# Performance work log

Measured on AMD Instinct MI355X. Metric: run time of the kernel, lower is better.

Reference implementation:

```python
import jax, jax.numpy as jnp
import numpy as np

N, T, S, A, L, Z = 128, 100, 128, 32, 1024, 1024


def _gru(x, h0, Wih, Whh, bih, bhh):
    # x: [T, N, in], h0: [N, H]; torch nn.GRU cell math
    xg = jnp.einsum('tni,gi->tng', x, Wih) + bih  # [T, N, 3H]

    def step(h, xg_t):
        hg = h @ Whh.T + bhh
        xr, xz, xn = jnp.split(xg_t, 3, axis=-1)
        hr, hz, hn = jnp.split(hg, 3, axis=-1)
        r = jax.nn.sigmoid(xr + hr)
        z = jax.nn.sigmoid(xz + hz)
        n = jnp.tanh(xn + r * hn)
        h_new = (1.0 - z) * n + z * h
        return h_new, h_new

    hT, out = jax.lax.scan(step, h0, xg)
    return out, hT  # out: [T, N, H]


def _roll_batch(x, shifts):
    # per-sample left-roll along time: out[n, t] = x[n, (t + shifts[n]) % T]
    Tt = x.shape[1]
    idx = (jnp.arange(Tt)[None, :] + shifts[:, None]) % Tt  # [N, T]
    return jnp.take_along_axis(x, idx[:, :, None], axis=1)


def setup_inputs() -> dict:
    key = jax.random.key(0)
    ks = jax.random.split(key, 40)
    # ragged valid lengths in [50, 98]; zero tails trigger split-point detection
    lengths = jax.random.randint(ks[0], (N,), 50, 99)
    s = jax.random.normal(ks[1], (N, T, S), jnp.float32)
    valid = (jnp.arange(T)[None, :] < lengths[:, None])[:, :, None]
    s = jnp.where(valid, s, 0.0)
    inp = {
        's': s,
        'a': jax.random.normal(ks[2], (N, T, A), jnp.float32),
        's_final': jax.random.normal(ks[3], (N, S), jnp.float32),
        's_next': jax.random.normal(ks[4], (N, T, S), jnp.float32),
        'eps': jax.random.normal(ks[5], (N, Z), jnp.float32),
    }
    shapes = {
        'enc_Wih': (3 * L, S + A), 'enc_Whh': (3 * L, L), 'enc_bih': (3 * L,), 'enc_bhh': (3 * L,),
        'mu_W': (Z, L), 'mu_b': (Z,), 'lv_W': (Z, L), 'lv_b': (Z,),
        'st1_W': (128, L), 'st1_b': (128,), 'st2_W': (64, 128), 'st2_b': (64,),
        'st3_W': (S, 64), 'st3_b': (S,),
        'dec_Wih': (3 * Z, A), 'dec_Whh': (3 * Z, Z), 'dec_bih': (3 * Z,), 'dec_bhh': (3 * Z,),
        'd1_W': (128, Z), 'd1_b': (128,), 'd2_W': (64, 128), 'd2_b': (64,),
        'd3_W': (S, 64), 'd3_b': (S,),
    }
    for i, (name, shp) in enumerate(shapes.items()):
        fan_in = shp[-1] if len(shp) > 1 else 1024
        bound = 1.0 / np.sqrt(fan_in)
        inp[name] = jax.random.uniform(ks[6 + i], shp, jnp.float32, -bound, bound)
    return inp


def reference(s, a, s_final, s_next, eps,
              enc_Wih, enc_Whh, enc_bih, enc_bhh,
              mu_W, mu_b, lv_W, lv_b,
              st1_W, st1_b, st2_W, st2_b, st3_W, st3_b,
              dec_Wih, dec_Whh, dec_bih, dec_bhh,
              d1_W, d1_b, d2_W, d2_b, d3_W, d3_b):
    Nn, Tt = s.shape[0], s.shape[1]
    # split points: first t where s[n, t+1] is all-zero (padding tail)
    is_zero = jnp.all(s == 0.0, axis=-1)                    # [N, T]
    end = jnp.argmax(is_zero[:, 1:], axis=1)                # end_points
    start = end + 2                                         # start_points
    # encoder (initial hidden = ones, per original)
    x = jnp.concatenate([s, a], axis=-1).transpose(1, 0, 2)  # [T, N, S+A]
    h0 = jnp.ones((Nn, enc_Whh.shape[-1]), dtype=s.dtype)
    enc_out, _ = _gru(x, h0, enc_Wih, enc_Whh, enc_bih, enc_bhh)  # [T, N, L]
    enc_out = enc_out.transpose(1, 0, 2)                          # [N, T, L]
    hf = jnp.take_along_axis(enc_out, end[:, None, None], axis=1)[:, 0, :]  # [N, L]
    # reparametrize
    mu = hf @ mu_W.T + mu_b
    logvar = hf @ lv_W.T + lv_b
    emb = mu + jnp.exp(logvar / 2.0) * eps
    # final-state head (computed but not used in the returned loss, per original)
    x1 = jax.nn.relu(emb @ st1_W.T + st1_b)
    x2 = jax.nn.relu(x1 @ st2_W.T + st2_b)
    s_final_hat = x2 @ st3_W.T + st3_b
    # decoder: per-sample roll of actions by -start, initial hidden = embeddings
    a_roll = _roll_batch(a, start)
    dec_out, _ = _gru(a_roll.transpose(1, 0, 2), emb, dec_Wih, dec_Whh, dec_bih, dec_bhh)  # [T, N, Z]
    y1 = jax.nn.relu(dec_out @ d1_W.T + d1_b)
    y2 = jax.nn.relu(y1 @ d2_W.T + d2_b)
    s_next_hat = (y2 @ d3_W.T + d3_b).transpose(1, 0, 2)    # [N, T, S]
    # masked L1 loss on rolled next-states: error[n, :T-start[n]]
    s_next_roll = _roll_batch(s_next, start)
    err = jnp.abs(s_next_roll - s_next_hat)
    mask = (jnp.arange(Tt)[None, :] < (Tt - start)[:, None]).astype(err.dtype)
    loss = jnp.sum(err * mask[:, :, None])
    return loss.reshape(1, 1)
```

## Files before the change

### kernel.cpp

```cpp
#include <hip/hip_runtime.h>
#include <math.h>

#define NN_ 128
#define TT  100
#define SS  128
#define AA  32
#define LL  1024
#define NBLK 256
#define HRS  1034


typedef __attribute__((ext_vector_type(8))) short bf16x8;
typedef __attribute__((ext_vector_type(4))) float f32x4;
typedef __attribute__((ext_vector_type(4))) int   i32x4;

__device__ __forceinline__ float sigmoidf_(float x) { return 1.0f / (1.0f + expf(-x)); }
__device__ __forceinline__ unsigned short f2bf(float x) {
    union { float f; unsigned u; } v; v.f = x;
    return (unsigned short)((v.u + 0x7fffu + ((v.u >> 16) & 1u)) >> 16);
}

__device__ __forceinline__ i32x4 ldg16(const unsigned short* p) {
    i32x4 r; asm volatile("global_load_dwordx4 %0, %1, off sc0 sc1"
                          : "=&v"(r) : "v"((unsigned long long)p));
    return r;
}
__device__ __forceinline__ void stg16(unsigned short* p, bf16x8 v) {
    union { bf16x8 h; i32x4 i; } u; u.h = v;
    asm volatile("global_store_dwordx4 %0, %1, off sc0 sc1"
                 :: "v"((unsigned long long)p), "v"(u.i) : "memory");
}
__device__ __forceinline__ void st2(unsigned short* p, unsigned short v) {
    asm volatile("global_store_short %0, %1, off sc0 sc1"
                 :: "v"((unsigned long long)p), "v"((unsigned)v) : "memory");
}
__device__ __forceinline__ int aload(const int* p) {
    return __hip_atomic_load(p, __ATOMIC_RELAXED, __HIP_MEMORY_SCOPE_AGENT);
}
__device__ __forceinline__ void astore(int* p, int v) {
    __hip_atomic_store(p, v, __ATOMIC_RELAXED, __HIP_MEMORY_SCOPE_AGENT);
}

struct PParams {
    const float *s, *a, *s_next, *eps;
    const float *eWih, *eWhh, *ebih, *ebhh;
    const float *muW, *mub, *lvW, *lvb;
    const float *dWih, *dWhh, *dbih, *dbhh;
    const float *d1W, *d1b, *d2W, *d2b, *d3W, *d3b;
    int *bar;
    int *endv, *startv, *limitv;
    unsigned short *hencAb, *hencBb, *hdecAb, *hdecBb, *hf_bf;
    unsigned short *eWih_b, *eWhh_b, *dWih_b, *dWhh_b, *mlW_b, *xenc_b, *adec_b;
    unsigned short *d1Wb, *d2Wb, *d3Wb;
    unsigned short *y1b, *y2b;
    float *loss;
};

__device__ __forceinline__ void stage_h32p(const unsigned short* __restrict__ src,
                                           const int* __restrict__ sperm,
                                           unsigned short* hstage, int tid) {
    i32x4 v[16];
    const int p = tid >> 7, col = (tid & 127) * 8;
    #pragma unroll
    for (int k = 0; k < 16; ++k) {
        const int row = sperm[p + 2 * k];
        v[k] = ldg16(src + (size_t)row * LL + col);
    }
    asm volatile("s_waitcnt vmcnt(0)" ::: "memory");
    #pragma unroll
    for (int k = 0; k < 16; ++k)
        *(i32x4*)&hstage[(p + 2 * k) * HRS + col] = v[k];
}

__device__ void gbar_global(int* bar, int bid, int tid, int gen) {
    __syncthreads();
    if (tid == 0) {
        if (aload(bar + 132) == 0) {
            const int g8 = bid & 7;
            int pos = __hip_atomic_fetch_add(bar + g8 * 16, 1, __ATOMIC_RELAXED, __HIP_MEMORY_SCOPE_AGENT);
            if (pos + 1 == (NBLK / 8) * gen) {
                int mp = __hip_atomic_fetch_add(bar + 128, 1, __ATOMIC_RELAXED, __HIP_MEMORY_SCOPE_AGENT);
                if (mp + 1 == 8 * gen) {
                    for (int b = 0; b < NBLK; ++b)
                        astore(bar + 144 + b * 16, gen);
                }
            }
            int it = 0;
            while (aload(bar + 144 + bid * 16) < gen) {
                __builtin_amdgcn_s_sleep(1);
                if (++it > 4000000) { astore(bar + 132, 1); break; }
            }
        }
    }
    __syncthreads();
}

__device__ void gbar_group(int* gb, int* brk, int lbid, int tid, int gen, int* sbrk) {
    asm volatile("s_waitcnt vmcnt(0)" ::: "memory");
    __syncthreads();
    if (tid == 0) {
        const int s = lbid & 3;
        int pos = __hip_atomic_fetch_add(gb + s * 16, 1, __ATOMIC_RELAXED, __HIP_MEMORY_SCOPE_AGENT);
        if (pos + 1 == 16 * gen) {
            int mp = __hip_atomic_fetch_add(gb + 64, 1, __ATOMIC_RELAXED, __HIP_MEMORY_SCOPE_AGENT);
            if (mp + 1 == 4 * gen)
                astore(gb + 80, gen);
        }
        if (*sbrk == 0) {
            int it = 0;
            while (aload(gb + 80) < gen) {
                __builtin_amdgcn_s_sleep(1);
                if (((++it) & 2047) == 0) {
                    if (aload(brk)) { *sbrk = 1; break; }
                    if (it > 2000000) { astore(brk, 1); *sbrk = 1; break; }
                }
            }
        }
    }
    __syncthreads();
}

__global__ void init_kernel(int* bar, float* loss) {
    for (int i = threadIdx.x; i < 5632; i += 256) bar[i] = 0;
    if (threadIdx.x == 0) loss[0] = 0.0f;
}

template<int XK, bool IS_DEC>
__device__ void gru_tile(const int* __restrict__ sperm, const int jb, const int tid,
    const unsigned short* __restrict__ h_bf, unsigned short* __restrict__ ho_bf,
    const unsigned short* __restrict__ Whh_b, const unsigned short* __restrict__ Wih_b,
    const unsigned short* __restrict__ x_bf,
    const float* __restrict__ bih, const float* __restrict__ bhh,
    const int* __restrict__ endv, unsigned short* __restrict__ hf_bf,
    int t, f32x4 (&red)[2][4][64], unsigned short* hstage, unsigned short* trb,
    f32x4& hold)
{
    const int lane = tid & 63, w = tid >> 6;
    const int nh = w & 1, kh = w >> 1;
    const int m = lane & 15, quad = lane >> 4;
    const int jcol = jb + m;

    stage_h32p(h_bf, sperm, hstage, tid);
    __syncthreads();

    f32x4 accr{}, accz{}, acchn{}, accxn{};

    {
        const int arow = (nh * 16 + m) * HRS + quad * 8;
        const unsigned short* brp = Whh_b + (size_t)(0 * LL + jcol) * LL + quad * 8;
        const unsigned short* bzp = Whh_b + (size_t)(1 * LL + jcol) * LL + quad * 8;
        const unsigned short* bnp = Whh_b + (size_t)(2 * LL + jcol) * LL + quad * 8;
        #pragma unroll 4
        for (int c = kh * 16; c < kh * 16 + 16; ++c) {
            const int k0 = c * 32;
            bf16x8 av = *(const bf16x8*)&hstage[arow + k0];
            bf16x8 br = *(const bf16x8*)(brp + k0);
            bf16x8 bz = *(const bf16x8*)(bzp + k0);
            bf16x8 bn = *(const bf16x8*)(bnp + k0);
            accr  = __builtin_amdgcn_mfma_f32_16x16x32_bf16(av, br, accr, 0, 0, 0);
            accz  = __builtin_amdgcn_mfma_f32_16x16x32_bf16(av, bz, accz, 0, 0, 0);
            acchn = __builtin_amdgcn_mfma_f32_16x16x32_bf16(av, bn, acchn, 0, 0, 0);
        }
    }
    {
        const int XC = XK / 32, XC0 = (XC + 1) / 2;
        const size_t xstride = IS_DEC ? (size_t)(50 * AA) : (size_t)(TT * (SS + AA));
        const int nphys = sperm[nh * 16 + m];
        const unsigned short* xp  = x_bf + (size_t)nphys * xstride + (size_t)t * XK + quad * 8;
        const unsigned short* brp = Wih_b + (size_t)(0 * LL + jcol) * XK + quad * 8;
        const unsigned short* bzp = Wih_b + (size_t)(1 * LL + jcol) * XK + quad * 8;
        const unsigned short* bnp = Wih_b + (size_t)(2 * LL + jcol) * XK + quad * 8;
        #pragma unroll
        for (int c = (kh ? XC0 : 0); c < (kh ? XC : XC0); ++c) {
            const int k0 = c * 32;
            bf16x8 av = *(const bf16x8*)(xp + k0);
            bf16x8 br = *(const bf16x8*)(brp + k0);
            bf16x8 bz = *(const bf16x8*)(bzp + k0);
            bf16x8 bn = *(const bf16x8*)(bnp + k0);
            accr  = __builtin_amdgcn_mfma_f32_16x16x32_bf16(av, br, accr, 0, 0, 0);
            accz  = __builtin_amdgcn_mfma_f32_16x16x32_bf16(av, bz, accz, 0, 0, 0);
            accxn = __builtin_amdgcn_mfma_f32_16x16x32_bf16(av, bn, accxn, 0, 0, 0);
        }
    }
    if (kh == 1) {
        red[nh][0][lane] = accr;  red[nh][1][lane] = accz;
        red[nh][2][lane] = acchn; red[nh][3][lane] = accxn;
    }
    __syncthreads();
    if (kh == 0) {
        accr  += red[nh][0][lane];  accz  += red[nh][1][lane];
        acchn += red[nh][2][lane];  accxn += red[nh][3][lane];
        const float br_  = bih[jcol] + bhh[jcol];
        const float bz_  = bih[LL + jcol] + bhh[LL + jcol];
        const float bxn_ = bih[2 * LL + jcol];
        const float bhn_ = bhh[2 * LL + jcol];
        unsigned short* tr = trb + nh * (16 * 24);
        #pragma unroll
        for (int i = 0; i < 4; ++i) {
            const int n = sperm[nh * 16 + quad * 4 + i];
            float r = sigmoidf_(accr[i] + br_);
            float z = sigmoidf_(accz[i] + bz_);
            float g = tanhf(accxn[i] + bxn_ + r * (acchn[i] + bhn_));
            float hn = (1.0f - z) * g + z * hold[i];
            hold[i] = hn;
            unsigned short hb = f2bf(hn);
            tr[(quad * 4 + i) * 24 + m] = hb;
            if (!IS_DEC) { if (endv[n] == t) st2(hf_bf + (size_t)n * LL + jcol, hb); }
        }
        if (lane < 32) {
            const int nl = lane >> 1, jh = lane & 1;
            bf16x8 vv = *(const bf16x8*)&tr[nl * 24 + jh * 8];
            stg16(ho_bf + (size_t)sperm[nh * 16 + nl] * LL + jb + jh * 8, vv);
        }
    }
}

__device__ void emb_tile(const PParams& P, const int* __restrict__ sperm, const int jb,
                         const int tid, f32x4 (&red)[2][4][64], unsigned short* hstage,
                         unsigned short* trb, f32x4& hold)
{
    const int lane = tid & 63, w = tid >> 6;
    const int nh = w & 1, kh = w >> 1;
    const int m = lane & 15, quad = lane >> 4;
    const int jcol = jb + m;

    stage_h32p(P.hf_bf, sperm, hstage, tid);
    __syncthreads();

    f32x4 accm{}, accl{};
    const int arow = (nh * 16 + m) * HRS + quad * 8;
    const unsigned short* bmp = P.mlW_b + (size_t)jcol * LL + quad * 8;
    const unsigned short* blp = P.mlW_b + (size_t)(LL + jcol) * LL + quad * 8;
    #pragma unroll 4
    for (int c = kh * 16; c < kh * 16 + 16; ++c) {
        const int k0 = c * 32;
        bf16x8 av = *(const bf16x8*)&hstage[arow + k0];
        bf16x8 bm = *(const bf16x8*)(bmp + k0);
        bf16x8 bl = *(const bf16x8*)(blp + k0);
        accm = __builtin_amdgcn_mfma_f32_16x16x32_bf16(av, bm, accm, 0, 0, 0);
        accl = __builtin_amdgcn_mfma_f32_16x16x32_bf16(av, bl, accl, 0, 0, 0);
    }
    if (kh == 1) { red[nh][0][lane] = accm; red[nh][1][lane] = accl; }
    __syncthreads();
    if (kh == 0) {
        accm += red[nh][0][lane]; accl += red[nh][1][lane];
        unsigned short* tr = trb + nh * (16 * 24);
        #pragma unroll
        for (int i = 0; i < 4; ++i) {
            const int n = sperm[nh * 16 + quad * 4 + i];
            float mu = accm[i] + P.mub[jcol];
            float lv = accl[i] + P.lvb[jcol];
            float e = mu + expf(0.5f * lv) * P.eps[(size_t)n * LL + jcol];
            hold[i] = e;
            tr[(quad * 4 + i) * 24 + m] = f2bf(e);
        }
        if (lane < 32) {
            const int nl = lane >> 1, jh = lane & 1;
            bf16x8 vv = *(const bf16x8*)&tr[nl * 24 + jh * 8];
            stg16(P.hdecAb + (size_t)sperm[nh * 16 + nl] * LL + jb + jh * 8, vv);
        }
    }
}

__device__ void y1_tile(const PParams& P, int t, int tid,
                        const unsigned short* __restrict__ hstage,
                        unsigned short* __restrict__ y1cur)
{
    if (tid >= 64) return;
    const int m16 = tid & 15, quad = tid >> 4;
    const int rb = (t & 1) * 16, cb = (t >> 1) * 16;
    f32x4 acc{};
    const int abase = (rb + m16) * HRS + quad * 8;
    const unsigned short* bp = P.d1Wb + (size_t)(cb + m16) * LL + quad * 8;
    #pragma unroll 4
    for (int ch = 0; ch < 32; ++ch) {
        bf16x8 av = *(const bf16x8*)&hstage[abase + ch * 32];
        bf16x8 bv = *(const bf16x8*)(bp + ch * 32);
        acc = __builtin_amdgcn_mfma_f32_16x16x32_bf16(av, bv, acc, 0, 0, 0);
    }
    const float b = P.d1b[cb + m16];
    #pragma unroll
    for (int i = 0; i < 4; ++i)
        st2(y1cur + (rb + quad * 4 + i) * 128 + cb + m16, f2bf(fmaxf(acc[i] + b, 0.0f)));
}
__device__ void y2_tile(const PParams& P, int t, int tid,
                        const unsigned short* __restrict__ y1prev,
                        unsigned short* __restrict__ y2cur)
{
    if (tid >= 64) return;
    const int m16 = tid & 15, quad = tid >> 4;
    const int rb = (t & 1) * 16, cb = (t >> 1) * 16;
    i32x4 a4[4];
    #pragma unroll
    for (int ch = 0; ch < 4; ++ch)
        a4[ch] = ldg16(y1prev + (size_t)(rb + m16) * 128 + ch * 32 + quad * 8);
    asm volatile("s_waitcnt vmcnt(0)" ::: "memory");
    f32x4 acc{};
    #pragma unroll
    for (int ch = 0; ch < 4; ++ch) {
        union { i32x4 i; bf16x8 h; } u; u.i = a4[ch];
        bf16x8 bv = *(const bf16x8*)(P.d2Wb + (size_t)(cb + m16) * 128 + ch * 32 + quad * 8);
        acc = __builtin_amdgcn_mfma_f32_16x16x32_bf16(u.h, bv, acc, 0, 0, 0);
    }
    const float b = P.d2b[cb + m16];
    #pragma unroll
    for (int i = 0; i < 4; ++i)
        st2(y2cur + (rb + quad * 4 + i) * 64 + cb + m16, f2bf(fmaxf(acc[i] + b, 0.0f)));
}
__device__ void y3_loss(const PParams& P, const int* __restrict__ sperm, int t, int tid,
                        const unsigned short* __restrict__ y2prev, int ti, float& lossacc)
{
    if (tid >= 64) return;
    const int m16 = tid & 15, quad = tid >> 4;
    const int rb = (t & 1) * 16, cb = (t >> 1) * 16;
    i32x4 a2[2];
    #pragma unroll
    for (int ch = 0; ch < 2; ++ch)
        a2[ch] = ldg16(y2prev + (size_t)(rb + m16) * 64 + ch * 32 + quad * 8);
    asm volatile("s_waitcnt vmcnt(0)" ::: "memory");
    f32x4 acc{};
    #pragma unroll
    for (int ch = 0; ch < 2; ++ch) {
        union { i32x4 i; bf16x8 h; } u; u.i = a2[ch];
        bf16x8 bv = *(const bf16x8*)(P.d3Wb + (size_t)(cb + m16) * 64 + ch * 32 + quad * 8);
        acc = __builtin_amdgcn_mfma_f32_16x16x32_bf16(u.h, bv, acc, 0, 0, 0);
    }
    const int col = cb + m16;
    const float b = P.d3b[col];
    #pragma unroll
    for (int i = 0; i < 4; ++i) {
        const int n = sperm[rb + quad * 4 + i];
        if (ti < P.limitv[n]) {
            int trw = ti + P.startv[n]; if (trw >= TT) trw -= TT;
            float v = P.s_next[(size_t)n * TT * SS + (size_t)trw * SS + col];
            lossacc += fabsf(v - (acc[i] + b));
        }
    }
}

__global__ __launch_bounds__(256, 2)
void persist(PParams P)
{
    __shared__ __align__(16) unsigned short hstage[32 * HRS];
    __shared__ __align__(16) char shu[9728];
    __shared__ int sperm[32];
    __shared__ int mint, sME, sML, sbrk;
    f32x4 (&red)[2][4][64] = *(f32x4 (*)[2][4][64])(shu);
    unsigned short* trb = (unsigned short*)(shu + 8192);
    const int bid = blockIdx.x, tid = threadIdx.x;
    const int g = bid & 3, lbid = bid >> 2;
    const int jb = lbid * 16;
    int* gb = P.bar + 4608 + g * 128;
    int* brk = P.bar + 132;

    {
        const long N0 = 3072L * 160, N1 = N0 + 3072L * 1024, N2 = N1 + 3072L * 32,
                   N3 = N2 + 3072L * 1024, N4 = N3 + 1048576L, N5 = N4 + 1048576L,
                   N6 = N5 + 128L * 100 * 160, N7 = N6 + 131072L, N8 = N7 + 8192L,
                   N9 = N8 + 8192L;
        for (long i = (long)bid * 256 + tid; i < N9; i += (long)NBLK * 256) {
            if (i < N0)      P.eWih_b[i]      = f2bf(P.eWih[i]);
            else if (i < N1) P.eWhh_b[i - N0] = f2bf(P.eWhh[i - N0]);
            else if (i < N2) P.dWih_b[i - N1] = f2bf(P.dWih[i - N1]);
            else if (i < N3) P.dWhh_b[i - N2] = f2bf(P.dWhh[i - N2]);
            else if (i < N4) P.mlW_b[i - N3]  = f2bf(P.muW[i - N3]);
            else if (i < N5) P.mlW_b[1048576L + (i - N4)] = f2bf(P.lvW[i - N4]);
            else if (i < N6) {
                long j = i - N5;
                int  k = (int)(j % 160);
                long nt = j / 160;
                int  t = (int)(nt % 100), n = (int)(nt / 100);
                float v = (k < SS) ? P.s[(size_t)n * TT * SS + (size_t)t * SS + k]
                                   : P.a[(size_t)n * TT * AA + (size_t)t * AA + (k - SS)];
                P.xenc_b[j] = f2bf(v);
            }
            else if (i < N7) P.d1Wb[i - N6] = f2bf(P.d1W[i - N6]);
            else if (i < N8) P.d2Wb[i - N7] = f2bf(P.d2W[i - N7]);
            else             P.d3Wb[i - N8] = f2bf(P.d3W[i - N8]);
        }
    }
    if (bid < NN_) {
        const int n = bid;
        if (tid == 0) mint = TT - 1;
        __syncthreads();
        int t = tid + 1;
        if (t < TT && tid < 128) {
            const float* row = P.s + (size_t)n * TT * SS + (size_t)t * SS;
            bool allz = true;
            for (int i = 0; i < SS; ++i) { if (row[i] != 0.0f) { allz = false; break; } }
            if (allz) atomicMin(&mint, t);
        }
        __syncthreads();
        const int m = mint, st = m + 1;
        if (tid == 0) { P.endv[n] = m - 1; P.startv[n] = st; P.limitv[n] = TT - 1 - m; }
        for (int idx = tid; idx < LL; idx += 256)
            P.hencAb[(size_t)n * LL + idx] = 0x3F80;
        for (int idx = tid; idx < 50 * AA; idx += 256) {
            int i = idx >> 5, k = idx & 31;
            int tr = i + st; if (tr >= TT) tr -= TT;
            P.adec_b[(size_t)n * (50 * AA) + idx] =
                f2bf(P.a[(size_t)n * TT * AA + (size_t)tr * AA + k]);
        }
    }
    __syncthreads();
    if (tid == 0) __threadfence();
    gbar_global(P.bar, bid, tid, 1);
    if (tid == 0) __threadfence();
    __syncthreads();

    {
        int* keys = (int*)shu;
        if (tid < 128) keys[tid] = P.endv[tid];
        if (tid == 0) sbrk = 0;
        __syncthreads();
        if (tid < 128) {
            const int k = keys[tid];
            int r = 0;
            for (int j = 0; j < 128; ++j) {
                const int kj = keys[j];
                r += (kj < k) | ((kj == k) & (j < tid));
            }
            if (r >= g * 32 && r < g * 32 + 32) sperm[r - g * 32] = tid;
        }
        __syncthreads();
    }

    int ME, ML;
    {
        int lv = 0, ev = 0;
        if (tid < 32) { const int n = sperm[tid]; lv = P.limitv[n]; ev = P.endv[n]; }
        if (tid < 64) {
            for (int off = 16; off >= 1; off >>= 1) {
                lv = max(lv, __shfl_down(lv, off));
                ev = max(ev, __shfl_down(ev, off));
            }
            if (tid == 0) { sML = lv; sME = ev; }
        }
        __syncthreads();
        ML = sML; ME = sME;
        __syncthreads();
    }

    f32x4 hold = { 1.0f, 1.0f, 1.0f, 1.0f };
    float lossacc = 0.0f;
    int ggen = 0;

    for (int t = 0; t <= ME; ++t) {
        const unsigned short* hib = (t & 1) ? P.hencBb : P.hencAb;
        unsigned short*       hob = (t & 1) ? P.hencAb : P.hencBb;
        gru_tile<160, false>(sperm, jb, tid, hib, hob,
                             P.eWhh_b, P.eWih_b, P.xenc_b, P.ebih, P.ebhh,
                             P.endv, P.hf_bf, t, red, hstage, trb, hold);
        gbar_group(gb, brk, lbid, tid, ++ggen, &sbrk);
    }

    emb_tile(P, sperm, jb, tid, red, hstage, trb, hold);
    gbar_group(gb, brk, lbid, tid, ++ggen, &sbrk);

    unsigned short* y1g = P.y1b + (size_t)g * 2 * 32 * 128;
    unsigned short* y2g = P.y2b + (size_t)g * 2 * 32 * 64;
    for (int i = 0; i <= ML + 2; ++i) {
        const unsigned short* hib = (i & 1) ? P.hdecBb : P.hdecAb;
        if (i < ML) {
            unsigned short* hob = (i & 1) ? P.hdecAb : P.hdecBb;
            gru_tile<32, true>(sperm, jb, tid, hib, hob,
                               P.dWhh_b, P.dWih_b, P.adec_b, P.dbih, P.dbhh,
                               nullptr, nullptr, i, red, hstage, trb, hold);
        } else if (i == ML && lbid >= 48) {
            stage_h32p(hib, sperm, hstage, tid);
            __syncthreads();
        }
        if (lbid >= 48) {
            if (i >= 1 && i <= ML)
                y1_tile(P, lbid - 48, tid, hstage, y1g + (size_t)(i & 1) * 32 * 128);
        } else if (lbid >= 32 && lbid < 40) {
            if (i >= 2 && i <= ML + 1)
                y2_tile(P, lbid - 32, tid, y1g + (size_t)((i & 1) ^ 1) * 32 * 128,
                        y2g + (size_t)(i & 1) * 32 * 64);
        } else if (lbid < 16) {
            if (i >= 3)
                y3_loss(P, sperm, lbid, tid, y2g + (size_t)((i & 1) ^ 1) * 32 * 64,
                        i - 3, lossacc);
        }
        gbar_group(gb, brk, lbid, tid, ++ggen, &sbrk);
    }

    if (lbid < 16 && tid < 64) {
        for (int off = 32; off >= 1; off >>= 1) lossacc += __shfl_down(lossacc, off);
        if (tid == 0) atomicAdd(P.loss, lossacc);
    }
}

extern "C" void kernel_launch(void* const* d_in, const int* in_sizes, int n_in,
                              void* d_out, int out_size, void* d_ws, size_t ws_size,
                              hipStream_t stream) {
    PParams P;
    P.s      = (const float*)d_in[0];
    P.a      = (const float*)d_in[1];
    P.s_next = (const float*)d_in[3];
    P.eps    = (const float*)d_in[4];
    P.eWih   = (const float*)d_in[5];
    P.eWhh   = (const float*)d_in[6];
    P.ebih   = (const float*)d_in[7];
    P.ebhh   = (const float*)d_in[8];
    P.muW    = (const float*)d_in[9];
    P.mub    = (const float*)d_in[10];
    P.lvW    = (const float*)d_in[11];
    P.lvb    = (const float*)d_in[12];
    P.dWih   = (const float*)d_in[19];
    P.dWhh   = (const float*)d_in[20];
    P.dbih   = (const float*)d_in[21];
    P.dbhh   = (const float*)d_in[22];
    P.d1W    = (const float*)d_in[23];
    P.d1b    = (const float*)d_in[24];
    P.d2W    = (const float*)d_in[25];
    P.d2b    = (const float*)d_in[26];
    P.d3W    = (const float*)d_in[27];
    P.d3b    = (const float*)d_in[28];
    P.loss   = (float*)d_out;

    char* p = (char*)d_ws;
    P.bar    = (int*)p;                    p += 24576;
    P.endv   = (int*)p;                    p += 512;
    P.startv = (int*)p;                    p += 512;
    P.limitv = (int*)p;                    p += 512;
    p += 2560;
    P.hencAb = (unsigned short*)p;         p += 128 * 1024 * 2;
    P.hencBb = (unsigned short*)p;         p += 128 * 1024 * 2;
    P.hdecAb = (unsigned short*)p;         p += 128 * 1024 * 2;
    P.hdecBb = (unsigned short*)p;         p += 128 * 1024 * 2;
    P.hf_bf  = (unsigned short*)p;         p += 128 * 1024 * 2;
    P.eWih_b = (unsigned short*)p;         p += 3072 * 160 * 2;
    P.eWhh_b = (unsigned short*)p;         p += 3072 * 1024 * 2;
    P.dWih_b = (unsigned short*)p;         p += 3072 * 32 * 2;
    P.dWhh_b = (unsigned short*)p;         p += 3072 * 1024 * 2;
    P.mlW_b  = (unsigned short*)p;         p += 2048 * 1024 * 2;
    P.xenc_b = (unsigned short*)p;         p += 128 * 100 * 160 * 2;
    P.adec_b = (unsigned short*)p;         p += 128 * 50 * 32 * 2;
    P.d1Wb   = (unsigned short*)p;         p += 128 * 1024 * 2;
    P.d2Wb   = (unsigned short*)p;         p += 64 * 128 * 2;
    P.d3Wb   = (unsigned short*)p;         p += 128 * 64 * 2;
    P.y1b    = (unsigned short*)p;         p += 4 * 2 * 32 * 128 * 2;
    P.y2b    = (unsigned short*)p;         p += 4 * 2 * 32 * 64 * 2;

    hipLaunchKernelGGL(init_kernel, dim3(1), dim3(256), 0, stream, P.bar, P.loss);
    hipLaunchKernelGGL(persist, dim3(NBLK), dim3(256), 0, stream, P);
}
```

Measured before the change: 1.760 ms.

## Split grid barrier and overlap next-step input projection with barrier wait

The group barrier is split into separate arrive and wait phases. The input-to-hidden MFMA projection for the next timestep now runs between them, taking it off the serial recurrent critical path. The projection results are carried in registers and used as the starting accumulators for the hidden-state matmul. Scheduling barriers are also added after load waits in the y-tiles. The cost is extra live registers and possible register pressure.

Result: faster. 1.643 ms (-6.6%).

```diff
diff --git a/kernel.cpp b/kernel.cpp
--- a/kernel.cpp
+++ b/kernel.cpp
@@ -95,7 +95,7 @@
     __syncthreads();
 }
 
-__device__ void gbar_group(int* gb, int* brk, int lbid, int tid, int gen, int* sbrk) {
+__device__ void gbar_arrive(int* gb, int lbid, int tid, int gen) {
     asm volatile("s_waitcnt vmcnt(0)" ::: "memory");
     __syncthreads();
     if (tid == 0) {
@@ -106,14 +106,16 @@
             if (mp + 1 == 4 * gen)
                 astore(gb + 80, gen);
         }
-        if (*sbrk == 0) {
-            int it = 0;
-            while (aload(gb + 80) < gen) {
-                __builtin_amdgcn_s_sleep(1);
-                if (((++it) & 2047) == 0) {
-                    if (aload(brk)) { *sbrk = 1; break; }
-                    if (it > 2000000) { astore(brk, 1); *sbrk = 1; break; }
-                }
+    }
+}
+__device__ void gbar_wait(int* gb, int* brk, int tid, int gen, int* sbrk) {
+    if (tid == 0 && *sbrk == 0) {
+        int it = 0;
+        while (aload(gb + 80) < gen) {
+            __builtin_amdgcn_s_sleep(1);
+            if (((++it) & 2047) == 0) {
+                if (aload(brk)) { *sbrk = 1; break; }
+                if (it > 2000000) { astore(brk, 1); *sbrk = 1; break; }
             }
         }
     }
@@ -126,24 +128,53 @@
 }
 
 template<int XK, bool IS_DEC>
-__device__ void gru_tile(const int* __restrict__ sperm, const int jb, const int tid,
-    const unsigned short* __restrict__ h_bf, unsigned short* __restrict__ ho_bf,
-    const unsigned short* __restrict__ Whh_b, const unsigned short* __restrict__ Wih_b,
-    const unsigned short* __restrict__ x_bf,
-    const float* __restrict__ bih, const float* __restrict__ bhh,
-    const int* __restrict__ endv, unsigned short* __restrict__ hf_bf,
-    int t, f32x4 (&red)[2][4][64], unsigned short* hstage, unsigned short* trb,
-    f32x4& hold)
+__device__ __forceinline__ void x_part(const PParams& P, const int* __restrict__ sperm,
+    const int jb, const int tid, int t, f32x4& axr, f32x4& axz, f32x4& axn)
 {
     const int lane = tid & 63, w = tid >> 6;
     const int nh = w & 1, kh = w >> 1;
     const int m = lane & 15, quad = lane >> 4;
     const int jcol = jb + m;
+    const unsigned short* Wih_b = IS_DEC ? P.dWih_b : P.eWih_b;
+    const unsigned short* x_bf  = IS_DEC ? P.adec_b : P.xenc_b;
+    f32x4 r{}, z{}, n{};
+    const int XC = XK / 32, XC0 = (XC + 1) / 2;
+    const size_t xstride = IS_DEC ? (size_t)(50 * AA) : (size_t)(TT * (SS + AA));
+    const unsigned short* xp  = x_bf + (size_t)sperm[nh * 16 + m] * xstride + (size_t)t * XK + quad * 8;
+    const unsigned short* brp = Wih_b + (size_t)(0 * LL + jcol) * XK + quad * 8;
+    const unsigned short* bzp = Wih_b + (size_t)(1 * LL + jcol) * XK + quad * 8;
+    const unsigned short* bnp = Wih_b + (size_t)(2 * LL + jcol) * XK + quad * 8;
+    #pragma unroll
+    for (int c = (kh ? XC0 : 0); c < (kh ? XC : XC0); ++c) {
+        const int k0 = c * 32;
+        bf16x8 av = *(const bf16x8*)(xp + k0);
+        bf16x8 br = *(const bf16x8*)(brp + k0);
+        bf16x8 bz = *(const bf16x8*)(bzp + k0);
+        bf16x8 bn = *(const bf16x8*)(bnp + k0);
+        r = __builtin_amdgcn_mfma_f32_16x16x32_bf16(av, br, r, 0, 0, 0);
+        z = __builtin_amdgcn_mfma_f32_16x16x32_bf16(av, bz, z, 0, 0, 0);
+        n = __builtin_amdgcn_mfma_f32_16x16x32_bf16(av, bn, n, 0, 0, 0);
+    }
+    axr = r; axz = z; axn = n;
+}
+
+template<bool IS_DEC>
+__device__ void gru_tile(const PParams& P, const int* __restrict__ sperm, const int jb,
+    const int tid, const unsigned short* __restrict__ h_bf,
+    unsigned short* __restrict__ ho_bf, const unsigned short* __restrict__ Whh_b,
+    const float* __restrict__ bih, const float* __restrict__ bhh, int t,
+    f32x4 (&red)[2][4][64], unsigned short* hstage, unsigned short* trb, f32x4& hold,
+    const f32x4 axr, const f32x4 axz, const f32x4 axn)
+{
+    const int lane = tid & 63, w = tid >> 6;
+    const int nh = w & 1, kh = w >> 1;
+    const int m = lane & 15, quad = lane >> 4;
+    const int jcol = jb + m;
 
     stage_h32p(h_bf, sperm, hstage, tid);
     __syncthreads();
 
-    f32x4 accr{}, accz{}, acchn{}, accxn{};
+    f32x4 accr = axr, accz = axz, acchn{}, accxn = axn;
 
     {
         const int arow = (nh * 16 + m) * HRS + quad * 8;
@@ -160,26 +191,6 @@
             accr  = __builtin_amdgcn_mfma_f32_16x16x32_bf16(av, br, accr, 0, 0, 0);
             accz  = __builtin_amdgcn_mfma_f32_16x16x32_bf16(av, bz, accz, 0, 0, 0);
             acchn = __builtin_amdgcn_mfma_f32_16x16x32_bf16(av, bn, acchn, 0, 0, 0);
-        }
-    }
-    {
-        const int XC = XK / 32, XC0 = (XC + 1) / 2;
-        const size_t xstride = IS_DEC ? (size_t)(50 * AA) : (size_t)(TT * (SS + AA));
-        const int nphys = sperm[nh * 16 + m];
-        const unsigned short* xp  = x_bf + (size_t)nphys * xstride + (size_t)t * XK + quad * 8;
-        const unsigned short* brp = Wih_b + (size_t)(0 * LL + jcol) * XK + quad * 8;
-        const unsigned short* bzp = Wih_b + (size_t)(1 * LL + jcol) * XK + quad * 8;
-        const unsigned short* bnp = Wih_b + (size_t)(2 * LL + jcol) * XK + quad * 8;
-        #pragma unroll
-        for (int c = (kh ? XC0 : 0); c < (kh ? XC : XC0); ++c) {
-            const int k0 = c * 32;
-            bf16x8 av = *(const bf16x8*)(xp + k0);
-            bf16x8 br = *(const bf16x8*)(brp + k0);
-            bf16x8 bz = *(const bf16x8*)(bzp + k0);
-            bf16x8 bn = *(const bf16x8*)(bnp + k0);
-            accr  = __builtin_amdgcn_mfma_f32_16x16x32_bf16(av, br, accr, 0, 0, 0);
-            accz  = __builtin_amdgcn_mfma_f32_16x16x32_bf16(av, bz, accz, 0, 0, 0);
-            accxn = __builtin_amdgcn_mfma_f32_16x16x32_bf16(av, bn, accxn, 0, 0, 0);
         }
     }
     if (kh == 1) {
@@ -205,7 +216,7 @@
             hold[i] = hn;
             unsigned short hb = f2bf(hn);
             tr[(quad * 4 + i) * 24 + m] = hb;
-            if (!IS_DEC) { if (endv[n] == t) st2(hf_bf + (size_t)n * LL + jcol, hb); }
+            if (!IS_DEC) { if (P.endv[n] == t) st2(P.hf_bf + (size_t)n * LL + jcol, hb); }
         }
         if (lane < 32) {
             const int nl = lane >> 1, jh = lane & 1;
@@ -295,6 +306,7 @@
     for (int ch = 0; ch < 4; ++ch)
         a4[ch] = ldg16(y1prev + (size_t)(rb + m16) * 128 + ch * 32 + quad * 8);
     asm volatile("s_waitcnt vmcnt(0)" ::: "memory");
+    __builtin_amdgcn_sched_barrier(0);
     f32x4 acc{};
     #pragma unroll
     for (int ch = 0; ch < 4; ++ch) {
@@ -318,6 +330,7 @@
     for (int ch = 0; ch < 2; ++ch)
         a2[ch] = ldg16(y2prev + (size_t)(rb + m16) * 64 + ch * 32 + quad * 8);
     asm volatile("s_waitcnt vmcnt(0)" ::: "memory");
+    __builtin_amdgcn_sched_barrier(0);
     f32x4 acc{};
     #pragma unroll
     for (int ch = 0; ch < 2; ++ch) {
@@ -442,20 +455,27 @@
     }
 
     f32x4 hold = { 1.0f, 1.0f, 1.0f, 1.0f };
+    f32x4 axr{}, axz{}, axn{};
     float lossacc = 0.0f;
     int ggen = 0;
 
+    x_part<160, false>(P, sperm, jb, tid, 0, axr, axz, axn);
     for (int t = 0; t <= ME; ++t) {
         const unsigned short* hib = (t & 1) ? P.hencBb : P.hencAb;
         unsigned short*       hob = (t & 1) ? P.hencAb : P.hencBb;
-        gru_tile<160, false>(sperm, jb, tid, hib, hob,
-                             P.eWhh_b, P.eWih_b, P.xenc_b, P.ebih, P.ebhh,
-                             P.endv, P.hf_bf, t, red, hstage, trb, hold);
-        gbar_group(gb, brk, lbid, tid, ++ggen, &sbrk);
+        gru_tile<false>(P, sperm, jb, tid, hib, hob, P.eWhh_b, P.ebih, P.ebhh,
+                        t, red, hstage, trb, hold, axr, axz, axn);
+        ++ggen;
+        gbar_arrive(gb, lbid, tid, ggen);
+        if (t < ME) x_part<160, false>(P, sperm, jb, tid, t + 1, axr, axz, axn);
+        gbar_wait(gb, brk, tid, ggen, &sbrk);
     }
 
     emb_tile(P, sperm, jb, tid, red, hstage, trb, hold);
-    gbar_group(gb, brk, lbid, tid, ++ggen, &sbrk);
+    ++ggen;
+    gbar_arrive(gb, lbid, tid, ggen);
+    x_part<32, true>(P, sperm, jb, tid, 0, axr, axz, axn);
+    gbar_wait(gb, brk, tid, ggen, &sbrk);
 
     unsigned short* y1g = P.y1b + (size_t)g * 2 * 32 * 128;
     unsigned short* y2g = P.y2b + (size_t)g * 2 * 32 * 64;
@@ -463,9 +483,8 @@
         const unsigned short* hib = (i & 1) ? P.hdecBb : P.hdecAb;
         if (i < ML) {
             unsigned short* hob = (i & 1) ? P.hdecAb : P.hdecBb;
-            gru_tile<32, true>(sperm, jb, tid, hib, hob,
-                               P.dWhh_b, P.dWih_b, P.adec_b, P.dbih, P.dbhh,
-                               nullptr, nullptr, i, red, hstage, trb, hold);
+            gru_tile<true>(P, sperm, jb, tid, hib, hob, P.dWhh_b, P.dbih, P.dbhh,
+                           i, red, hstage, trb, hold, axr, axz, axn);
         } else if (i == ML && lbid >= 48) {
             stage_h32p(hib, sperm, hstage, tid);
             __syncthreads();
@@ -482,7 +501,10 @@
                 y3_loss(P, sperm, lbid, tid, y2g + (size_t)((i & 1) ^ 1) * 32 * 64,
                         i - 3, lossacc);
         }
-        gbar_group(gb, brk, lbid, tid, ++ggen, &sbrk);
+        ++ggen;
+        gbar_arrive(gb, lbid, tid, ggen);
+        if (i + 1 < ML) x_part<32, true>(P, sperm, jb, tid, i + 1, axr, axz, axn);
+        gbar_wait(gb, brk, tid, ggen, &sbrk);
     }
 
     if (lbid < 16 && tid < 64) {
```
